# Optimization experiments

Hardware: AMD Instinct MI355X
Metric: run time of the kernel (lower is better)

The kernel has to match this reference:

```python
import jax, jax.numpy as jnp
import numpy as np

# BCQLinear packed forward: weight[o, i] reconstructed from per-(out,group,bit)
# alpha scales and +/-1 binary codes via einsum('oib,oiab->oia'), then a plain
# out-channel-wise matmul (in_ch_wise=False) plus bias. beta is NOT used in the
# packed forward path of the original module.

B, S = 2, 1024          # token dims (m...)
O = 4096                 # out_features
G, A, NB = 32, 128, 3    # n_groups, group_size, n_bits; in_features = G*A = 4096


def setup_inputs() -> dict:
    key = jax.random.key(0)
    k1, k2, k3, k4 = jax.random.split(key, 4)
    x = jax.random.normal(k1, (B, S, G * A), dtype=jnp.float32)
    # binary codes are strictly +/-1 (Packer.unpack yields sign bits)
    b = jnp.sign(jax.random.normal(k2, (O, G, A, NB)))
    binary = jnp.where(b == 0, 1.0, b).astype(jnp.float32)
    # alpha scales are small positive magnitudes in practice
    alpha = jax.random.uniform(k3, (O, G, NB), dtype=jnp.float32,
                               minval=0.01, maxval=0.1)
    bias = 0.01 * jax.random.normal(k4, (O,), dtype=jnp.float32)
    return {"input": x, "binary": binary, "alpha": alpha, "bias": bias}


def reference(input, binary, alpha, bias):
    # dequantize: [O, G, A] -> [O, I]
    weight = jnp.einsum('oib,oiab->oia', alpha, binary).reshape(binary.shape[0], -1)
    # out-channel-wise matmul: m...i, oi -> m...o
    out = jnp.einsum('msi,oi->mso', input, weight) + bias
    return out
```

## Files before the change

kernel.cpp:

```cpp
#include <hip/hip_runtime.h>
#include <hip/hip_bf16.h>
#include <stdint.h>

typedef __bf16 bf16x8 __attribute__((ext_vector_type(8)));
typedef float  f32x4  __attribute__((ext_vector_type(4)));

static constexpr int Mdim = 2048;
static constexpr int Ndim = 4096;
static constexpr int Kdim = 4096;
static constexpr int DQ_BLOCKS = (Ndim * Kdim / 8) / 256;
static constexpr int CVT_BLOCKS = (Mdim * Kdim / 8) / 256;

__global__ __launch_bounds__(256)
void prep(const float* __restrict__ binary, const float* __restrict__ alpha,
          const float* __restrict__ x, __bf16* __restrict__ w,
          __bf16* __restrict__ xb) {
  const int b = blockIdx.x;
  if (b < DQ_BLOCKS) {
    long e = ((long)b * 256 + threadIdx.x) * 8;
    int o = (int)(e >> 12);
    int g = (int)((e & 4095) >> 7);
    const float* al = alpha + ((long)o * 32 + g) * 3;
    float a0 = al[0], a1 = al[1], a2 = al[2];
    const float4* q = (const float4*)(binary + e * 3);
    float4 q0 = q[0], q1 = q[1], q2 = q[2], q3 = q[3], q4 = q[4], q5 = q[5];
    bf16x8 wv;
    wv[0] = (__bf16)(a0 * q0.x + a1 * q0.y + a2 * q0.z);
    wv[1] = (__bf16)(a0 * q0.w + a1 * q1.x + a2 * q1.y);
    wv[2] = (__bf16)(a0 * q1.z + a1 * q1.w + a2 * q2.x);
    wv[3] = (__bf16)(a0 * q2.y + a1 * q2.z + a2 * q2.w);
    wv[4] = (__bf16)(a0 * q3.x + a1 * q3.y + a2 * q3.z);
    wv[5] = (__bf16)(a0 * q3.w + a1 * q4.x + a2 * q4.y);
    wv[6] = (__bf16)(a0 * q4.z + a1 * q4.w + a2 * q5.x);
    wv[7] = (__bf16)(a0 * q5.y + a1 * q5.z + a2 * q5.w);
    *(bf16x8*)(w + e) = wv;
  } else {
    long e = ((long)(b - DQ_BLOCKS) * 256 + threadIdx.x) * 8;
    float4 v0 = *(const float4*)(x + e);
    float4 v1 = *(const float4*)(x + e + 4);
    bf16x8 r;
    r[0] = (__bf16)v0.x; r[1] = (__bf16)v0.y; r[2] = (__bf16)v0.z; r[3] = (__bf16)v0.w;
    r[4] = (__bf16)v1.x; r[5] = (__bf16)v1.y; r[6] = (__bf16)v1.z; r[7] = (__bf16)v1.w;
    *(bf16x8*)(xb + e) = r;
  }
}

static constexpr int NT = Kdim / 64;
static constexpr int BUF = 49152;

__device__ __forceinline__ void g2l16(const void* g, void* l) {
  __builtin_amdgcn_global_load_lds(
      (const __attribute__((address_space(1))) void*)g,
      (__attribute__((address_space(3))) void*)l, 16, 0, 0);
}

#define BAR()    __builtin_amdgcn_s_barrier()
#define LGKM0()  asm volatile("s_waitcnt lgkmcnt(0)" ::: "memory")
#define SCHED0() __builtin_amdgcn_sched_barrier(0)
#define VMC6()   asm volatile("s_waitcnt vmcnt(6)" ::: "memory")
#define VMC0()   asm volatile("s_waitcnt vmcnt(0)" ::: "memory")

#define STAGE_A(t, bo) do { \
  _Pragma("unroll") for (int j_ = 0; j_ < 2; ++j_) \
    g2l16(baseA[j_] + (t) * 64, sm + (bo) + (w * 2 + j_) * 1024); \
} while (0)
#define STAGE_B(t, bo) do { \
  _Pragma("unroll") for (int j_ = 0; j_ < 4; ++j_) \
    g2l16(baseB[j_] + (t) * 64, sm + (bo) + 16384 + (w * 4 + j_) * 1024); \
} while (0)

#define LOAD_A4(dst, bo) do { \
  _Pragma("unroll") for (int m_ = 0; m_ < 4; ++m_) \
    _Pragma("unroll") for (int h_ = 0; h_ < 2; ++h_) \
      dst[m_][h_] = *(const bf16x8*)(sm + (bo) + aoffbase + m_ * 2048 + swz[h_]); \
} while (0)
#define LOAD_B2(dst, bo, n0_) do { \
  _Pragma("unroll") for (int n_ = 0; n_ < 2; ++n_) \
    _Pragma("unroll") for (int h_ = 0; h_ < 2; ++h_) \
      dst[n_][h_] = *(const bf16x8*)(sm + (bo) + boffbase + ((n0_) + n_) * 2048 + swz[h_]); \
} while (0)

#define MMA16(fa_, fb_, n0_) do { \
  __builtin_amdgcn_s_setprio(1); \
  _Pragma("unroll") for (int m_ = 0; m_ < 4; ++m_) \
    _Pragma("unroll") for (int n_ = 0; n_ < 2; ++n_) { \
      acc[m_][(n0_) + n_] = __builtin_amdgcn_mfma_f32_16x16x32_bf16( \
          fa_[m_][0], fb_[n_][0], acc[m_][(n0_) + n_], 0, 0, 0); \
      acc[m_][(n0_) + n_] = __builtin_amdgcn_mfma_f32_16x16x32_bf16( \
          fa_[m_][1], fb_[n_][1], acc[m_][(n0_) + n_], 0, 0, 0); \
    } \
  __builtin_amdgcn_s_setprio(0); \
} while (0)

__global__ __launch_bounds__(512, 2)
void gemm4(const __bf16* __restrict__ A, const __bf16* __restrict__ Bw,
           const float* __restrict__ bias, float* __restrict__ out) {
  __shared__ __align__(128) char sm[3 * BUF];
  const int tid = threadIdx.x, lane = tid & 63, w = tid >> 6;
  const int wm = w >> 2, wn = w & 3;

  const int bid = blockIdx.x;
  const int logical = (bid & 7) * 32 + (bid >> 3);
  const int tm = logical & 15;
  const int tn = logical >> 4;

  const int rlo = lane >> 3;
  const int gsw = (lane & 7) ^ rlo;
  const __bf16* baseA[2];
  const __bf16* baseB[4];
#pragma unroll
  for (int j = 0; j < 2; ++j)
    baseA[j] = A + (long)(tm * 128 + w * 16 + j * 8 + rlo) * Kdim + gsw * 8;
#pragma unroll
  for (int j = 0; j < 4; ++j)
    baseB[j] = Bw + (long)(tn * 256 + w * 32 + j * 8 + rlo) * Kdim + gsw * 8;

  int swz[2];
#pragma unroll
  for (int h = 0; h < 2; ++h)
    swz[h] = (((h * 4 + (lane >> 4)) ^ (lane & 7)) << 4);
  const int aoffbase = (wm * 64 + (lane & 15)) * 128;
  const int boffbase = 16384 + (wn * 64 + (lane & 15)) * 128;

  f32x4 acc[4][4] = {};

  STAGE_A(0, 0);   STAGE_B(0, 0);
  STAGE_A(1, BUF); STAGE_B(1, BUF);
  VMC6();
  BAR();

  bf16x8 fa[4][2], fb01[2][2], fb23[2][2];
  int ba = 0, bb = BUF, bc = 2 * BUF;

  for (int t = 0; t < NT; ++t) {
    const bool pf = (t + 2 < NT);
    LOAD_A4(fa, ba);
    LOAD_B2(fb01, ba, 0);
    if (pf) STAGE_A(t + 2, bc);
    BAR(); LGKM0(); SCHED0();
    MMA16(fa, fb01, 0);
    BAR();
    LOAD_B2(fb23, ba, 2);
    if (pf) STAGE_B(t + 2, bc);
    if (t < NT - 2) { VMC6(); } else { VMC0(); }
    BAR(); LGKM0(); SCHED0();
    MMA16(fa, fb23, 2);
    BAR();
    int tmp = ba; ba = bb; bb = bc; bc = tmp;
  }

  float* lf = (float*)sm;
  const int r4 = (lane >> 4) * 4;
  const int cl = lane & 15;
#pragma unroll
  for (int m = 0; m < 4; ++m)
#pragma unroll
    for (int n = 0; n < 4; ++n)
#pragma unroll
      for (int r = 0; r < 4; ++r) {
        int row = wm * 64 + m * 16 + r4 + r;
        int col = wn * 64 + n * 16 + cl;
        lf[row * 260 + col] = acc[m][n][r];
      }
  __syncthreads();
#pragma unroll
  for (int i = 0; i < 16; ++i) {
    int idx = tid + i * 512;
    int row = idx >> 6;
    int c4 = idx & 63;
    f32x4 v = *(const f32x4*)(lf + row * 260 + c4 * 4);
    float4 bv = *(const float4*)(bias + tn * 256 + c4 * 4);
    v[0] += bv.x; v[1] += bv.y; v[2] += bv.z; v[3] += bv.w;
    *(f32x4*)(out + (long)(tm * 128 + row) * Ndim + tn * 256 + c4 * 4) = v;
  }
}

extern "C" void kernel_launch(void* const* d_in, const int* in_sizes, int n_in,
                              void* d_out, int out_size, void* d_ws, size_t ws_size,
                              hipStream_t stream) {
  const float* x      = (const float*)d_in[0];
  const float* binary = (const float*)d_in[1];
  const float* alpha  = (const float*)d_in[2];
  const float* bias   = (const float*)d_in[3];
  float* out = (float*)d_out;

  __bf16* wb = (__bf16*)d_ws;
  __bf16* xb = wb + (size_t)Ndim * Kdim;

  prep<<<dim3(DQ_BLOCKS + CVT_BLOCKS), 256, 0, stream>>>(binary, alpha, x, wb, xb);
  gemm4<<<dim3(256), 512, 0, stream>>>(xb, wb, bias, out);
}
```

Measured before the change: 120.7 us.

## Overlap weight dequantization of later K-chunks with GEMM via cross-block counters

```diff
diff --git a/kernel.cpp b/kernel.cpp
--- a/kernel.cpp
+++ b/kernel.cpp
@@ -8,21 +8,23 @@
 static constexpr int Mdim = 2048;
 static constexpr int Ndim = 4096;
 static constexpr int Kdim = 4096;
-static constexpr int DQ_BLOCKS = (Ndim * Kdim / 8) / 256;
+static constexpr int KC   = 1024;
+static constexpr int DQ0_BLOCKS = (Ndim * KC / 8) / 256;
 static constexpr int CVT_BLOCKS = (Mdim * Kdim / 8) / 256;
 
 __global__ __launch_bounds__(256)
-void prep(const float* __restrict__ binary, const float* __restrict__ alpha,
-          const float* __restrict__ x, __bf16* __restrict__ w,
-          __bf16* __restrict__ xb) {
+void prep0(const float* __restrict__ binary, const float* __restrict__ alpha,
+           const float* __restrict__ x, __bf16* __restrict__ w,
+           __bf16* __restrict__ xb, unsigned int* __restrict__ ctr) {
   const int b = blockIdx.x;
-  if (b < DQ_BLOCKS) {
+  if (b == 0 && threadIdx.x < 4) ctr[threadIdx.x] = 0;
+  if (b < DQ0_BLOCKS) {
     long e = ((long)b * 256 + threadIdx.x) * 8;
-    int o = (int)(e >> 12);
-    int g = (int)((e & 4095) >> 7);
-    const float* al = alpha + ((long)o * 32 + g) * 3;
+    int row = (int)(e >> 10);
+    int colc = (int)(e & 1023);
+    const float* al = alpha + ((long)row * 32 + (colc >> 7)) * 3;
     float a0 = al[0], a1 = al[1], a2 = al[2];
-    const float4* q = (const float4*)(binary + e * 3);
+    const float4* q = (const float4*)(binary + ((long)row * Kdim + colc) * 3);
     float4 q0 = q[0], q1 = q[1], q2 = q[2], q3 = q[3], q4 = q[4], q5 = q[5];
     bf16x8 wv;
     wv[0] = (__bf16)(a0 * q0.x + a1 * q0.y + a2 * q0.z);
@@ -33,9 +35,9 @@
     wv[5] = (__bf16)(a0 * q3.w + a1 * q4.x + a2 * q4.y);
     wv[6] = (__bf16)(a0 * q4.z + a1 * q4.w + a2 * q5.x);
     wv[7] = (__bf16)(a0 * q5.y + a1 * q5.z + a2 * q5.w);
-    *(bf16x8*)(w + e) = wv;
+    *(bf16x8*)(w + (long)row * Kdim + colc) = wv;
   } else {
-    long e = ((long)(b - DQ_BLOCKS) * 256 + threadIdx.x) * 8;
+    long e = ((long)(b - DQ0_BLOCKS) * 256 + threadIdx.x) * 8;
     float4 v0 = *(const float4*)(x + e);
     float4 v1 = *(const float4*)(x + e + 4);
     bf16x8 r;
@@ -45,7 +47,6 @@
   }
 }
 
-static constexpr int NT = Kdim / 64;
 static constexpr int BUF = 49152;
 
 __device__ __forceinline__ void g2l16(const void* g, void* l) {
@@ -57,8 +58,7 @@
 #define BAR()    __builtin_amdgcn_s_barrier()
 #define LGKM0()  asm volatile("s_waitcnt lgkmcnt(0)" ::: "memory")
 #define SCHED0() __builtin_amdgcn_sched_barrier(0)
-#define VMC6()   asm volatile("s_waitcnt vmcnt(6)" ::: "memory")
-#define VMC0()   asm volatile("s_waitcnt vmcnt(0)" ::: "memory")
+#define GATE(n)  asm volatile("s_waitcnt vmcnt(" #n ")" ::: "memory")
 
 #define STAGE_A(t, bo) do { \
   _Pragma("unroll") for (int j_ = 0; j_ < 2; ++j_) \
@@ -92,14 +92,66 @@
   __builtin_amdgcn_s_setprio(0); \
 } while (0)
 
+#define ISSUE_A(cn_, tq_) do { \
+  long wf_ = (((long)(tq_) * 256 + bid) * 512 + tid) * 8; \
+  int row_ = (int)(wf_ >> 10); \
+  int col_ = (cn_) * 1024 + (int)(wf_ & 1023); \
+  dq_b = binary + ((long)row_ * Kdim + col_) * 3; \
+  dq_w = Bw + (long)row_ * Kdim + col_; \
+  dq_a = alpha + ((long)row_ * 32 + (col_ >> 7)) * 3; \
+  asm volatile("global_load_dwordx4 %0, %1, off"           : "=v"(q0) : "v"(dq_b) : "memory"); \
+  asm volatile("global_load_dwordx4 %0, %1, off offset:16" : "=v"(q1) : "v"(dq_b) : "memory"); \
+  asm volatile("global_load_dwordx4 %0, %1, off offset:32" : "=v"(q2) : "v"(dq_b) : "memory"); \
+  asm volatile("global_load_dword %0, %1, off"             : "=v"(a0) : "v"(dq_a) : "memory"); \
+  asm volatile("global_load_dword %0, %1, off offset:4"    : "=v"(a1) : "v"(dq_a) : "memory"); \
+  asm volatile("global_load_dword %0, %1, off offset:8"    : "=v"(a2) : "v"(dq_a) : "memory"); \
+} while (0)
+#define ISSUE_B() do { \
+  asm volatile("global_load_dwordx4 %0, %1, off offset:48" : "=v"(q3) : "v"(dq_b) : "memory"); \
+  asm volatile("global_load_dwordx4 %0, %1, off offset:64" : "=v"(q4) : "v"(dq_b) : "memory"); \
+  asm volatile("global_load_dwordx4 %0, %1, off offset:80" : "=v"(q5) : "v"(dq_b) : "memory"); \
+} while (0)
+#define CONSUME(g_) do { \
+  GATE(g_); SCHED0(); \
+  bf16x8 wv_; \
+  wv_[0] = (__bf16)(a0 * q0.x + a1 * q0.y + a2 * q0.z); \
+  wv_[1] = (__bf16)(a0 * q0.w + a1 * q1.x + a2 * q1.y); \
+  wv_[2] = (__bf16)(a0 * q1.z + a1 * q1.w + a2 * q2.x); \
+  wv_[3] = (__bf16)(a0 * q2.y + a1 * q2.z + a2 * q2.w); \
+  wv_[4] = (__bf16)(a0 * q3.x + a1 * q3.y + a2 * q3.z); \
+  wv_[5] = (__bf16)(a0 * q3.w + a1 * q4.x + a2 * q4.y); \
+  wv_[6] = (__bf16)(a0 * q4.z + a1 * q4.w + a2 * q5.x); \
+  wv_[7] = (__bf16)(a0 * q5.y + a1 * q5.z + a2 * q5.w); \
+  *(bf16x8*)dq_w = wv_; \
+} while (0)
+
+#define TILE(tg_, PF_, PRE_, POST_, GATE_STMT) do { \
+  PRE_ \
+  LOAD_A4(fa, ba); LOAD_B2(fb01, ba, 0); \
+  if (PF_) STAGE_A((tg_) + 2, bc); \
+  BAR(); LGKM0(); SCHED0(); \
+  MMA16(fa, fb01, 0); \
+  BAR(); \
+  LOAD_B2(fb23, ba, 2); \
+  if (PF_) STAGE_B((tg_) + 2, bc); \
+  POST_ \
+  GATE_STMT; \
+  BAR(); LGKM0(); SCHED0(); \
+  MMA16(fa, fb23, 2); \
+  BAR(); \
+  { int tmp_ = ba; ba = bb; bb = bc; bc = tmp_; } \
+} while (0)
+
 __global__ __launch_bounds__(512, 2)
-void gemm4(const __bf16* __restrict__ A, const __bf16* __restrict__ Bw,
-           const float* __restrict__ bias, float* __restrict__ out) {
+void gemm5(const __bf16* __restrict__ A, __bf16* __restrict__ Bw,
+           const float* __restrict__ bias, float* __restrict__ out,
+           const float* __restrict__ binary, const float* __restrict__ alpha,
+           unsigned int* __restrict__ ctr) {
   __shared__ __align__(128) char sm[3 * BUF];
   const int tid = threadIdx.x, lane = tid & 63, w = tid >> 6;
   const int wm = w >> 2, wn = w & 3;
-
   const int bid = blockIdx.x;
+
   const int logical = (bid & 7) * 32 + (bid >> 3);
   const int tm = logical & 15;
   const int tn = logical >> 4;
@@ -123,30 +175,64 @@
   const int boffbase = 16384 + (wn * 64 + (lane & 15)) * 128;
 
   f32x4 acc[4][4] = {};
-
-  STAGE_A(0, 0);   STAGE_B(0, 0);
-  STAGE_A(1, BUF); STAGE_B(1, BUF);
-  VMC6();
-  BAR();
-
   bf16x8 fa[4][2], fb01[2][2], fb23[2][2];
   int ba = 0, bb = BUF, bc = 2 * BUF;
 
-  for (int t = 0; t < NT; ++t) {
-    const bool pf = (t + 2 < NT);
-    LOAD_A4(fa, ba);
-    LOAD_B2(fb01, ba, 0);
-    if (pf) STAGE_A(t + 2, bc);
-    BAR(); LGKM0(); SCHED0();
-    MMA16(fa, fb01, 0);
-    BAR();
-    LOAD_B2(fb23, ba, 2);
-    if (pf) STAGE_B(t + 2, bc);
-    if (t < NT - 2) { VMC6(); } else { VMC0(); }
-    BAR(); LGKM0(); SCHED0();
-    MMA16(fa, fb23, 2);
-    BAR();
-    int tmp = ba; ba = bb; bb = bc; bc = tmp;
+  const float* dq_b; const float* dq_a; __bf16* dq_w;
+  float4 q0, q1, q2, q3, q4, q5; float a0, a1, a2;
+
+  for (int c = 0; c < 4; ++c) {
+    if (c > 0) {
+      BAR();
+      if (tid == 0) {
+        while (__hip_atomic_load(&ctr[c], __ATOMIC_ACQUIRE, __HIP_MEMORY_SCOPE_AGENT) < 256u)
+          __builtin_amdgcn_s_sleep(4);
+      }
+      BAR();
+    }
+    const int tg0 = c * 16;
+    STAGE_A(tg0, ba); STAGE_B(tg0, ba);
+    STAGE_A(tg0 + 1, bb); STAGE_B(tg0 + 1, bb);
+    GATE(6); BAR();
+
+    if (c < 3) {
+      const int cn = c + 1;
+      TILE(tg0 + 0,  1, , ISSUE_A(cn, 0);, GATE(12));
+      TILE(tg0 + 1,  1, , ISSUE_B();,      GATE(15));
+      TILE(tg0 + 2,  1, ,               ,  GATE(9));
+      TILE(tg0 + 3,  1, CONSUME(6);, ,     GATE(7));
+      TILE(tg0 + 4,  1, , ISSUE_A(cn, 1);, GATE(12));
+      TILE(tg0 + 5,  1, , ISSUE_B();,      GATE(15));
+      TILE(tg0 + 6,  1, ,               ,  GATE(9));
+      TILE(tg0 + 7,  1, CONSUME(6);, ,     GATE(7));
+      TILE(tg0 + 8,  1, , ISSUE_A(cn, 2);, GATE(12));
+      TILE(tg0 + 9,  1, , ISSUE_B();,      GATE(15));
+      TILE(tg0 + 10, 1, ,               ,  GATE(9));
+      TILE(tg0 + 11, 1, CONSUME(6);, ,     GATE(7));
+      TILE(tg0 + 12, 1, , ISSUE_A(cn, 3);, GATE(12));
+      TILE(tg0 + 13, 1, , ISSUE_B();,      GATE(15));
+      TILE(tg0 + 14, 0, ,               ,  GATE(3));
+      TILE(tg0 + 15, 0, CONSUME(0);, ,     GATE(0));
+      if (tid == 0)
+        __hip_atomic_fetch_add(&ctr[c + 1], 1u, __ATOMIC_RELEASE, __HIP_MEMORY_SCOPE_AGENT);
+    } else {
+      TILE(tg0 + 0,  1, , , GATE(6));
+      TILE(tg0 + 1,  1, , , GATE(6));
+      TILE(tg0 + 2,  1, , , GATE(6));
+      TILE(tg0 + 3,  1, , , GATE(6));
+      TILE(tg0 + 4,  1, , , GATE(6));
+      TILE(tg0 + 5,  1, , , GATE(6));
+      TILE(tg0 + 6,  1, , , GATE(6));
+      TILE(tg0 + 7,  1, , , GATE(6));
+      TILE(tg0 + 8,  1, , , GATE(6));
+      TILE(tg0 + 9,  1, , , GATE(6));
+      TILE(tg0 + 10, 1, , , GATE(6));
+      TILE(tg0 + 11, 1, , , GATE(6));
+      TILE(tg0 + 12, 1, , , GATE(6));
+      TILE(tg0 + 13, 1, , , GATE(6));
+      TILE(tg0 + 14, 0, , , GATE(0));
+      TILE(tg0 + 15, 0, , , GATE(0));
+    }
   }
 
   float* lf = (float*)sm;
@@ -186,7 +272,8 @@
 
   __bf16* wb = (__bf16*)d_ws;
   __bf16* xb = wb + (size_t)Ndim * Kdim;
-
-  prep<<<dim3(DQ_BLOCKS + CVT_BLOCKS), 256, 0, stream>>>(binary, alpha, x, wb, xb);
-  gemm4<<<dim3(256), 512, 0, stream>>>(xb, wb, bias, out);
-}
+  unsigned int* ctr = (unsigned int*)(xb + (size_t)Mdim * Kdim);
+
+  prep0<<<dim3(DQ0_BLOCKS + CVT_BLOCKS), 256, 0, stream>>>(binary, alpha, x, wb, xb, ctr);
+  gemm5<<<dim3(256), 512, 0, stream>>>(xb, wb, bias, out, binary, alpha, ctr);
+}
```

Result: slower. 278.2 us (+130.4%).

## Prepack dequantized weights in MFMA fragment order and load B directly to registers

Applied to the files above, without the earlier changes.

```diff
diff --git a/kernel.cpp b/kernel.cpp
--- a/kernel.cpp
+++ b/kernel.cpp
@@ -8,21 +8,29 @@
 static constexpr int Mdim = 2048;
 static constexpr int Ndim = 4096;
 static constexpr int Kdim = 4096;
-static constexpr int DQ_BLOCKS = (Ndim * Kdim / 8) / 256;
+static constexpr int NT   = 64;
+static constexpr int WPK_BLOCKS = 8192;
 static constexpr int CVT_BLOCKS = (Mdim * Kdim / 8) / 256;
 
 __global__ __launch_bounds__(256)
 void prep(const float* __restrict__ binary, const float* __restrict__ alpha,
-          const float* __restrict__ x, __bf16* __restrict__ w,
+          const float* __restrict__ x, __bf16* __restrict__ wp,
           __bf16* __restrict__ xb) {
   const int b = blockIdx.x;
-  if (b < DQ_BLOCKS) {
-    long e = ((long)b * 256 + threadIdx.x) * 8;
-    int o = (int)(e >> 12);
-    int g = (int)((e & 4095) >> 7);
-    const float* al = alpha + ((long)o * 32 + g) * 3;
+  const int t = threadIdx.x;
+  if (b < WPK_BLOCKS) {
+    const int pack = b * 4 + (t >> 6);
+    const int lane = t & 63;
+    const int h  = pack & 1;
+    const int nf = (pack >> 1) & 3;
+    const int wn = (pack >> 3) & 3;
+    const int tt = (pack >> 5) & 63;
+    const int tn = pack >> 11;
+    const int o  = tn * 256 + wn * 64 + nf * 16 + (lane & 15);
+    const int k0 = tt * 64 + h * 32 + (lane >> 4) * 8;
+    const float* al = alpha + ((long)o * 32 + (k0 >> 7)) * 3;
     float a0 = al[0], a1 = al[1], a2 = al[2];
-    const float4* q = (const float4*)(binary + e * 3);
+    const float4* q = (const float4*)(binary + ((long)o * Kdim + k0) * 3);
     float4 q0 = q[0], q1 = q[1], q2 = q[2], q3 = q[3], q4 = q[4], q5 = q[5];
     bf16x8 wv;
     wv[0] = (__bf16)(a0 * q0.x + a1 * q0.y + a2 * q0.z);
@@ -33,9 +41,9 @@
     wv[5] = (__bf16)(a0 * q3.w + a1 * q4.x + a2 * q4.y);
     wv[6] = (__bf16)(a0 * q4.z + a1 * q4.w + a2 * q5.x);
     wv[7] = (__bf16)(a0 * q5.y + a1 * q5.z + a2 * q5.w);
-    *(bf16x8*)(w + e) = wv;
+    *(bf16x8*)(wp + (long)pack * 512 + lane * 8) = wv;
   } else {
-    long e = ((long)(b - DQ_BLOCKS) * 256 + threadIdx.x) * 8;
+    long e = ((long)(b - WPK_BLOCKS) * 256 + t) * 8;
     float4 v0 = *(const float4*)(x + e);
     float4 v1 = *(const float4*)(x + e + 4);
     bf16x8 r;
@@ -44,9 +52,6 @@
     *(bf16x8*)(xb + e) = r;
   }
 }
-
-static constexpr int NT = Kdim / 64;
-static constexpr int BUF = 49152;
 
 __device__ __forceinline__ void g2l16(const void* g, void* l) {
   __builtin_amdgcn_global_load_lds(
@@ -57,45 +62,43 @@
 #define BAR()    __builtin_amdgcn_s_barrier()
 #define LGKM0()  asm volatile("s_waitcnt lgkmcnt(0)" ::: "memory")
 #define SCHED0() __builtin_amdgcn_sched_barrier(0)
-#define VMC6()   asm volatile("s_waitcnt vmcnt(6)" ::: "memory")
-#define VMC0()   asm volatile("s_waitcnt vmcnt(0)" ::: "memory")
+#define GATE2()  asm volatile("s_waitcnt vmcnt(2)" ::: "memory")
+#define GATE0()  asm volatile("s_waitcnt vmcnt(0)" ::: "memory")
 
-#define STAGE_A(t, bo) do { \
+#define STAGE_A(t_, bo) do { \
   _Pragma("unroll") for (int j_ = 0; j_ < 2; ++j_) \
-    g2l16(baseA[j_] + (t) * 64, sm + (bo) + (w * 2 + j_) * 1024); \
-} while (0)
-#define STAGE_B(t, bo) do { \
-  _Pragma("unroll") for (int j_ = 0; j_ < 4; ++j_) \
-    g2l16(baseB[j_] + (t) * 64, sm + (bo) + 16384 + (w * 4 + j_) * 1024); \
+    g2l16(baseA[j_] + (long)(t_) * 64, sm + (bo) + (w * 2 + j_) * 1024); \
 } while (0)
 
-#define LOAD_A4(dst, bo) do { \
+#define LOAD_A(dst, bo) do { \
   _Pragma("unroll") for (int m_ = 0; m_ < 4; ++m_) \
     _Pragma("unroll") for (int h_ = 0; h_ < 2; ++h_) \
       dst[m_][h_] = *(const bf16x8*)(sm + (bo) + aoffbase + m_ * 2048 + swz[h_]); \
 } while (0)
-#define LOAD_B2(dst, bo, n0_) do { \
-  _Pragma("unroll") for (int n_ = 0; n_ < 2; ++n_) \
+
+#define LOADB(dst, t_) do { \
+  const __bf16* p_ = pBw + (size_t)(t_) * 16384; \
+  _Pragma("unroll") for (int n_ = 0; n_ < 4; ++n_) \
     _Pragma("unroll") for (int h_ = 0; h_ < 2; ++h_) \
-      dst[n_][h_] = *(const bf16x8*)(sm + (bo) + boffbase + ((n0_) + n_) * 2048 + swz[h_]); \
+      dst[n_][h_] = *(const bf16x8*)(p_ + (n_ * 2 + h_) * 512); \
 } while (0)
 
-#define MMA16(fa_, fb_, n0_) do { \
+#define MMA32(fa_, fb_) do { \
   __builtin_amdgcn_s_setprio(1); \
   _Pragma("unroll") for (int m_ = 0; m_ < 4; ++m_) \
-    _Pragma("unroll") for (int n_ = 0; n_ < 2; ++n_) { \
-      acc[m_][(n0_) + n_] = __builtin_amdgcn_mfma_f32_16x16x32_bf16( \
-          fa_[m_][0], fb_[n_][0], acc[m_][(n0_) + n_], 0, 0, 0); \
-      acc[m_][(n0_) + n_] = __builtin_amdgcn_mfma_f32_16x16x32_bf16( \
-          fa_[m_][1], fb_[n_][1], acc[m_][(n0_) + n_], 0, 0, 0); \
+    _Pragma("unroll") for (int n_ = 0; n_ < 4; ++n_) { \
+      acc[m_][n_] = __builtin_amdgcn_mfma_f32_16x16x32_bf16( \
+          fa_[m_][0], fb_[n_][0], acc[m_][n_], 0, 0, 0); \
+      acc[m_][n_] = __builtin_amdgcn_mfma_f32_16x16x32_bf16( \
+          fa_[m_][1], fb_[n_][1], acc[m_][n_], 0, 0, 0); \
     } \
   __builtin_amdgcn_s_setprio(0); \
 } while (0)
 
 __global__ __launch_bounds__(512, 2)
-void gemm4(const __bf16* __restrict__ A, const __bf16* __restrict__ Bw,
+void gemmB(const __bf16* __restrict__ A, const __bf16* __restrict__ Wp,
            const float* __restrict__ bias, float* __restrict__ out) {
-  __shared__ __align__(128) char sm[3 * BUF];
+  __shared__ __align__(128) char sm[147456];
   const int tid = threadIdx.x, lane = tid & 63, w = tid >> 6;
   const int wm = w >> 2, wn = w & 3;
 
@@ -107,46 +110,42 @@
   const int rlo = lane >> 3;
   const int gsw = (lane & 7) ^ rlo;
   const __bf16* baseA[2];
-  const __bf16* baseB[4];
 #pragma unroll
   for (int j = 0; j < 2; ++j)
     baseA[j] = A + (long)(tm * 128 + w * 16 + j * 8 + rlo) * Kdim + gsw * 8;
-#pragma unroll
-  for (int j = 0; j < 4; ++j)
-    baseB[j] = Bw + (long)(tn * 256 + w * 32 + j * 8 + rlo) * Kdim + gsw * 8;
 
   int swz[2];
 #pragma unroll
   for (int h = 0; h < 2; ++h)
     swz[h] = (((h * 4 + (lane >> 4)) ^ (lane & 7)) << 4);
   const int aoffbase = (wm * 64 + (lane & 15)) * 128;
-  const int boffbase = 16384 + (wn * 64 + (lane & 15)) * 128;
+
+  const __bf16* pBw = Wp + ((size_t)(tn * 2048 + wn * 8) * 512) + lane * 8;
 
   f32x4 acc[4][4] = {};
+  bf16x8 fa[4][2], fbX[4][2], fbY[4][2];
 
-  STAGE_A(0, 0);   STAGE_B(0, 0);
-  STAGE_A(1, BUF); STAGE_B(1, BUF);
-  VMC6();
-  BAR();
+  STAGE_A(0, 0);
+  LOADB(fbX, 0);
+  STAGE_A(1, 16384);
 
-  bf16x8 fa[4][2], fb01[2][2], fb23[2][2];
-  int ba = 0, bb = BUF, bc = 2 * BUF;
-
-  for (int t = 0; t < NT; ++t) {
-    const bool pf = (t + 2 < NT);
-    LOAD_A4(fa, ba);
-    LOAD_B2(fb01, ba, 0);
-    if (pf) STAGE_A(t + 2, bc);
-    BAR(); LGKM0(); SCHED0();
-    MMA16(fa, fb01, 0);
+  int bo0 = 0, bo1 = 16384, bo2 = 32768;
+  for (int i = 0; i < NT / 2; ++i) {
+    const int t0 = 2 * i, t1 = 2 * i + 1;
+    GATE2(); BAR();
+    LOAD_A(fa, bo0);
+    LOADB(fbY, t1);
+    if (t0 + 2 < NT) STAGE_A(t0 + 2, bo2);
+    LGKM0(); SCHED0();
+    MMA32(fa, fbX);
+    if (t1 == NT - 1) { GATE0(); } else { GATE2(); }
     BAR();
-    LOAD_B2(fb23, ba, 2);
-    if (pf) STAGE_B(t + 2, bc);
-    if (t < NT - 2) { VMC6(); } else { VMC0(); }
-    BAR(); LGKM0(); SCHED0();
-    MMA16(fa, fb23, 2);
-    BAR();
-    int tmp = ba; ba = bb; bb = bc; bc = tmp;
+    LOAD_A(fa, bo1);
+    if (t1 + 1 < NT) LOADB(fbX, t1 + 1);
+    if (t1 + 2 < NT) STAGE_A(t1 + 2, bo0);
+    LGKM0(); SCHED0();
+    MMA32(fa, fbY);
+    int tmp = bo0; bo0 = bo2; bo2 = bo1; bo1 = tmp;
   }
 
   float* lf = (float*)sm;
@@ -184,9 +183,9 @@
   const float* bias   = (const float*)d_in[3];
   float* out = (float*)d_out;
 
-  __bf16* wb = (__bf16*)d_ws;
-  __bf16* xb = wb + (size_t)Ndim * Kdim;
+  __bf16* wp = (__bf16*)d_ws;
+  __bf16* xb = wp + (size_t)Ndim * Kdim;
 
-  prep<<<dim3(DQ_BLOCKS + CVT_BLOCKS), 256, 0, stream>>>(binary, alpha, x, wb, xb);
-  gemm4<<<dim3(256), 512, 0, stream>>>(xb, wb, bias, out);
+  prep<<<dim3(WPK_BLOCKS + CVT_BLOCKS), 256, 0, stream>>>(binary, alpha, x, wp, xb);
+  gemmB<<<dim3(256), 512, 0, stream>>>(xb, wp, bias, out);
 }
```

New measurement: 134.1 us. +11.1%, slower.
